# Performance work log

Measured on AMD Instinct MI355X. Metric: run time of the kernel, lower is better.

## Reference

```python
import jax, jax.numpy as jnp
import numpy as np

D = 128
N_ROUNDS = 8


def _lin(k, fan_in, fan_out):
    return jax.random.normal(k, (fan_in, fan_out), jnp.float32) * (1.0 / np.sqrt(fan_in)).astype(np.float32)


def setup_inputs() -> dict:
    key = jax.random.key(0)
    ks = jax.random.split(key, 10)
    n_vars, n_clauses, n_edges = 65536, 262144, 1048576
    n_lits = 2 * n_vars
    clause_index = jax.random.randint(ks[0], (n_edges,), 0, n_clauses)
    literal_index = jax.random.randint(ks[1], (n_edges,), 0, n_lits)
    return {
        "n_vars": n_vars,
        "n_clauses": n_clauses,
        "clause_index": clause_index,
        "literal_index": literal_index,
        "L_init_scale": jnp.float32(1.0 / np.sqrt(D)),
        "C_init_scale": jnp.float32(1.0 / np.sqrt(D)),
        "LC_scale": jnp.float32(0.1),
        "CL_scale": jnp.float32(0.1),
        # C update MLP: [C, LC_msgs] (2d) -> d -> d
        "C_W1": _lin(ks[2], 2 * D, D), "C_b1": jnp.zeros((D,), jnp.float32),
        "C_W2": _lin(ks[3], D, D),     "C_b2": jnp.zeros((D,), jnp.float32),
        # L update MLP: [L, CL_msgs, flip(L)] (3d) -> d -> d
        "L_W1": _lin(ks[4], 3 * D, D), "L_b1": jnp.zeros((D,), jnp.float32),
        "L_W2": _lin(ks[5], D, D),     "L_b2": jnp.zeros((D,), jnp.float32),
        # V score MLP: [L_pos, L_neg] (2d) -> d -> 1
        "V_W1": _lin(ks[6], 2 * D, D), "V_b1": jnp.zeros((D,), jnp.float32),
        "V_W2": _lin(ks[7], D, 1),     "V_b2": jnp.zeros((1,), jnp.float32),
    }


def _mlp(x, W1, b1, W2, b2):
    # 2-layer MLP, relu on hidden layer only
    return jnp.maximum(x @ W1 + b1, 0.0) @ W2 + b2


def reference(n_vars, n_clauses, clause_index, literal_index,
              L_init_scale, C_init_scale, LC_scale, CL_scale,
              C_W1, C_b1, C_W2, C_b2,
              L_W1, L_b1, L_W2, L_b2,
              V_W1, V_b1, V_W2, V_b2):
    d = C_W2.shape[1]
    n_lits = 2 * n_vars
    L0 = jnp.ones((n_lits, d), jnp.float32) * L_init_scale
    C0 = jnp.ones((n_clauses, d), jnp.float32) * C_init_scale

    def flip(Lm):
        # swap positive/negative literal embeddings per variable
        pl, ul = jnp.split(Lm.reshape(n_vars, 2 * d), 2, axis=1)
        return jnp.concatenate([ul, pl], axis=1).reshape(n_lits, d)

    def step(carry, _):
        L, C = carry
        # literal -> clause messages (gather + segment sum)
        LC_msgs = jax.ops.segment_sum(L[literal_index], clause_index,
                                      num_segments=n_clauses) * LC_scale
        C_new = _mlp(jnp.concatenate([C, LC_msgs], axis=-1),
                     C_W1, C_b1, C_W2, C_b2) + C  # res_layers
        # clause -> literal messages
        CL_msgs = jax.ops.segment_sum(C_new[clause_index], literal_index,
                                      num_segments=n_lits) * CL_scale
        L_new = _mlp(jnp.concatenate([L, CL_msgs, flip(L)], axis=-1),
                     L_W1, L_b1, L_W2, L_b2) + L  # res_layers
        return (L_new, C_new), None

    (L, C), _ = jax.lax.scan(step, (L0, C0), None, length=N_ROUNDS)
    V = L.reshape(n_vars, 2 * d)
    V_scores = _mlp(V, V_W1, V_b1, V_W2, V_b2)
    return V_scores[:, 0]  # pi_core_var_logits
```

## Files before the change

kernel.cpp:

```cpp
#include <hip/hip_runtime.h>
#include <cstddef>

#define D_    128
#define NV_   65536
#define NL_   131072
#define NC_   262144
#define NE_   1048576
#define NROUNDS_ 8

typedef __attribute__((ext_vector_type(4)))  short short4v;
typedef __attribute__((ext_vector_type(8)))  short short8v;
typedef __attribute__((ext_vector_type(16))) float f32x16;

__device__ __forceinline__ float4 f4_load(const float* p) { return *(const float4*)p; }
__device__ __forceinline__ void   f4_store(float* p, float4 v) { *(float4*)p = v; }
__device__ __forceinline__ float4 f4_zero() { return make_float4(0.f, 0.f, 0.f, 0.f); }
__device__ __forceinline__ float4 f4_add(float4 a, float4 b) {
    a.x += b.x; a.y += b.y; a.z += b.z; a.w += b.w; return a;
}
__device__ __forceinline__ float4 f4_scale(float4 a, float s) {
    a.x *= s; a.y *= s; a.z *= s; a.w *= s; return a;
}

__device__ __forceinline__ void micro_fma(const float4 a[4], const float4 w[4], float4 acc[4]) {
#pragma unroll
    for (int i = 0; i < 4; i++) {
        float4 av = a[i];
        acc[i].x += av.x * w[0].x; acc[i].x += av.y * w[1].x; acc[i].x += av.z * w[2].x; acc[i].x += av.w * w[3].x;
        acc[i].y += av.x * w[0].y; acc[i].y += av.y * w[1].y; acc[i].y += av.z * w[2].y; acc[i].y += av.w * w[3].y;
        acc[i].z += av.x * w[0].z; acc[i].z += av.y * w[1].z; acc[i].z += av.z * w[2].z; acc[i].z += av.w * w[3].z;
        acc[i].w += av.x * w[0].w; acc[i].w += av.y * w[1].w; acc[i].w += av.z * w[2].w; acc[i].w += av.w * w[3].w;
    }
}

template<int KD, bool FLIP>
__device__ __forceinline__ void layer1_to_H(float* Xs, float* Wcs,
        const float* __restrict__ W1, const float* __restrict__ b1, int t)
{
    const int tr = t >> 5, tc = t & 31;
    float4 acc[4];
    acc[0] = acc[1] = acc[2] = acc[3] = f4_zero();
#pragma unroll 1
    for (int kc = 0; kc < KD; kc += 32) {
        __syncthreads();
#pragma unroll
        for (int i = t; i < 1024; i += 256)
            ((float4*)Wcs)[i] = ((const float4*)W1)[kc * 32 + i];
        __syncthreads();
        const bool fl = FLIP && (kc >= 256);
        const int ab = fl ? (kc - 256) : kc;
#pragma unroll
        for (int k = 0; k < 32; k += 4) {
            float4 a[4], w[4];
#pragma unroll
            for (int i = 0; i < 4; i++) {
                int r = 4 * tr + i;
                if (fl) r ^= 1;
                a[i] = f4_load(Xs + r * 256 + ab + k);
            }
#pragma unroll
            for (int kk = 0; kk < 4; kk++)
                w[kk] = f4_load(Wcs + (k + kk) * 128 + 4 * tc);
            micro_fma(a, w, acc);
        }
    }
    float4 bv = f4_load(b1 + 4 * tc);
    __syncthreads();
#pragma unroll
    for (int i = 0; i < 4; i++) {
        float4 h;
        h.x = fmaxf(acc[i].x + bv.x, 0.f);
        h.y = fmaxf(acc[i].y + bv.y, 0.f);
        h.z = fmaxf(acc[i].z + bv.z, 0.f);
        h.w = fmaxf(acc[i].w + bv.w, 0.f);
        f4_store(Xs + (4 * tr + i) * 256 + 128 + 4 * tc, h);
    }
}

__device__ __forceinline__ unsigned short f2bf(float x) {
    unsigned u = __float_as_uint(x);
    u += 0x7fffu + ((u >> 16) & 1u);
    return (unsigned short)(u >> 16);
}
__device__ __forceinline__ float bf2f(unsigned short h) {
    return __uint_as_float(((unsigned)h) << 16);
}
__device__ __forceinline__ void split_bf(float x, unsigned short& h, unsigned short& l) {
    h = f2bf(x);
    l = f2bf(x - bf2f(h));
}
__device__ __forceinline__ void cvt4(const float4& a, short4v& h, short4v& l) {
    unsigned short h0,h1,h2,h3,l0,l1,l2,l3;
    split_bf(a.x,h0,l0); split_bf(a.y,h1,l1); split_bf(a.z,h2,l2); split_bf(a.w,h3,l3);
    h = (short4v){(short)h0,(short)h1,(short)h2,(short)h3};
    l = (short4v){(short)l0,(short)l1,(short)l2,(short)l3};
}
__device__ __forceinline__ void cvt8(const float4& a, const float4& b, short8v& h, short8v& l) {
    unsigned short h0,h1,h2,h3,h4,h5,h6,h7,l0,l1,l2,l3,l4,l5,l6,l7;
    split_bf(a.x,h0,l0); split_bf(a.y,h1,l1); split_bf(a.z,h2,l2); split_bf(a.w,h3,l3);
    split_bf(b.x,h4,l4); split_bf(b.y,h5,l5); split_bf(b.z,h6,l6); split_bf(b.w,h7,l7);
    h = (short8v){(short)h0,(short)h1,(short)h2,(short)h3,(short)h4,(short)h5,(short)h6,(short)h7};
    l = (short8v){(short)l0,(short)l1,(short)l2,(short)l3,(short)l4,(short)l5,(short)l6,(short)l7};
}

__device__ __forceinline__ int pswz(int r, int k) { return (r * 256 + k * 2) ^ ((r & 7) << 4); }

__global__ void pack_weights(const float* __restrict__ W, short* __restrict__ out, int K)
{
    int o = blockIdx.x * 256 + threadIdx.x;
    if (o >= 2 * K * 128) return;
    int i = o & 7;
    int g = o >> 3;
    int n  = g & 127;
    int kk = (g >> 7) & 3;
    int p  = (g >> 9) & 1;
    int c  = g >> 10;
    int k  = c * 32 + kk * 8 + i;
    float x = W[k * 128 + n];
    unsigned short h = f2bf(x);
    unsigned short v = p ? f2bf(x - bf2f(h)) : h;
    out[o] = (short)v;
}

__global__ void fill_kernel(float* __restrict__ L, float* __restrict__ C,
                            const float* __restrict__ lsp, const float* __restrict__ csp)
{
    const float ls = *lsp, cs = *csp;
    const size_t stride = (size_t)gridDim.x * blockDim.x;
    size_t i0 = (size_t)blockIdx.x * blockDim.x + threadIdx.x;
    const size_t nL = (size_t)NL_ * D_ / 4, nC = (size_t)NC_ * D_ / 4;
    float4 lv = make_float4(ls, ls, ls, ls), cv = make_float4(cs, cs, cs, cs);
    for (size_t i = i0; i < nL; i += stride) ((float4*)L)[i] = lv;
    for (size_t i = i0; i < nC; i += stride) ((float4*)C)[i] = cv;
}

__global__ void count_kernel(const int* __restrict__ ci, const int* __restrict__ li,
                             int* __restrict__ ccnt, int* __restrict__ lcnt)
{
    int e = blockIdx.x * 256 + threadIdx.x;
    if (e < NE_) {
        atomicAdd(&ccnt[ci[e]], 1);
        atomicAdd(&lcnt[li[e]], 1);
    }
}

__global__ void scan_block(const int* __restrict__ in, int* __restrict__ out,
                           int* __restrict__ bsum)
{
    __shared__ int sh[256];
    const int t = threadIdx.x;
    const int base = blockIdx.x * 1024 + t * 4;
    int v0 = in[base], v1 = in[base + 1], v2 = in[base + 2], v3 = in[base + 3];
    int s = v0 + v1 + v2 + v3;
    sh[t] = s;
    __syncthreads();
    for (int off = 1; off < 256; off <<= 1) {
        int y = (t >= off) ? sh[t - off] : 0;
        __syncthreads();
        sh[t] += y;
        __syncthreads();
    }
    int excl = sh[t] - s;
    out[base + 0] = excl;
    out[base + 1] = excl + v0;
    out[base + 2] = excl + v0 + v1;
    out[base + 3] = excl + v0 + v1 + v2;
    if (t == 255) bsum[blockIdx.x] = sh[255];
}

__global__ void scan_top(int* __restrict__ bs, int n)
{
    __shared__ int sh[256];
    const int t = threadIdx.x;
    int v = (t < n) ? bs[t] : 0;
    sh[t] = v;
    __syncthreads();
    for (int off = 1; off < 256; off <<= 1) {
        int y = (t >= off) ? sh[t - off] : 0;
        __syncthreads();
        sh[t] += y;
        __syncthreads();
    }
    if (t < n) bs[t] = sh[t] - v;
}

__global__ void scan_add(int* __restrict__ offs, const int* __restrict__ bs,
                         int* __restrict__ cur, int n, int total)
{
    int i = blockIdx.x * 256 + threadIdx.x;
    if (i < n) {
        int v = offs[i] + bs[i >> 10];
        offs[i] = v;
        cur[i] = v;
    }
    if (i == 0) offs[n] = total;
}

__global__ void fill_csr(const int* __restrict__ ci, const int* __restrict__ li,
                         int* __restrict__ ccur, int* __restrict__ lcur,
                         int* __restrict__ cedges, int* __restrict__ ledges)
{
    int e = blockIdx.x * 256 + threadIdx.x;
    if (e < NE_) {
        int c = ci[e], l = li[e];
        int p = atomicAdd(&ccur[c], 1); cedges[p] = l;
        int q = atomicAdd(&lcur[l], 1); ledges[q] = c;
    }
}

template<bool FLIP>
__global__ __launch_bounds__(256, 5) void update_mfma(
        float* __restrict__ Mat, const float* __restrict__ Src,
        const int* __restrict__ offs, const int* __restrict__ eidx,
        const short* __restrict__ Wp1, const float* __restrict__ b1,
        const short* __restrict__ Wp2, const float* __restrict__ b2,
        const float* __restrict__ scale_p)
{
    __shared__ __align__(16) unsigned char SM[32768];
    unsigned char* sm = SM;
    const int t = threadIdx.x;
    const int base = blockIdx.x * 32;
    const int lane = t & 63, w = t >> 6;
    const int rA = lane & 31;
    const int kg = lane >> 5;
    const int nB = w * 32 + rA;

    float4 sv[4];
#pragma unroll
    for (int j = 0; j < 4; ++j)
        sv[j] = ((const float4*)Mat)[(size_t)base * 32 + t + j * 256];

    float4 a0 = f4_zero(), a1 = f4_zero(), a2 = f4_zero(), a3 = f4_zero();
    const int gr = t >> 3, gs = t & 7;
    {
        const int row = base + gr;
        const int e0 = offs[row], e1 = offs[row + 1];
        int e = e0;
        for (; e + 1 < e1; e += 2) {
            const float* P = Src + (size_t)eidx[e] * 128 + gs * 16;
            const float* Q = Src + (size_t)eidx[e + 1] * 128 + gs * 16;
            float4 p0 = f4_load(P), p1 = f4_load(P + 4), p2 = f4_load(P + 8), p3 = f4_load(P + 12);
            float4 q0 = f4_load(Q), q1 = f4_load(Q + 4), q2 = f4_load(Q + 8), q3 = f4_load(Q + 12);
            a0 = f4_add(a0, p0); a1 = f4_add(a1, p1); a2 = f4_add(a2, p2); a3 = f4_add(a3, p3);
            a0 = f4_add(a0, q0); a1 = f4_add(a1, q1); a2 = f4_add(a2, q2); a3 = f4_add(a3, q3);
        }
        if (e < e1) {
            const float* P = Src + (size_t)eidx[e] * 128 + gs * 16;
            a0 = f4_add(a0, f4_load(P));
            a1 = f4_add(a1, f4_load(P + 4));
            a2 = f4_add(a2, f4_load(P + 8));
            a3 = f4_add(a3, f4_load(P + 12));
        }
    }

#pragma unroll
    for (int j = 0; j < 4; ++j) {
        int i = t + j * 256;
        int r = i >> 5, q = i & 31;
        short4v hv, lv;
        cvt4(sv[j], hv, lv);
        *(short4v*)(sm + pswz(r, 4 * q)) = hv;
        *(short4v*)(sm + 8192 + pswz(r, 4 * q)) = lv;
    }
    {
        const float sc = *scale_p;
        a0 = f4_scale(a0, sc); a1 = f4_scale(a1, sc);
        a2 = f4_scale(a2, sc); a3 = f4_scale(a3, sc);
        short8v mh0, ml0, mh1, ml1;
        cvt8(a0, a1, mh0, ml0);
        cvt8(a2, a3, mh1, ml1);
        const int k0 = 16 * gs;
        *(short8v*)(sm + 16384 + pswz(gr, k0))     = mh0;
        *(short8v*)(sm + 16384 + pswz(gr, k0 + 8)) = mh1;
        *(short8v*)(sm + 24576 + pswz(gr, k0))     = ml0;
        *(short8v*)(sm + 24576 + pswz(gr, k0 + 8)) = ml1;
    }
    __syncthreads();

    f32x16 c0, c1;
#pragma unroll
    for (int i = 0; i < 16; ++i) { c0[i] = 0.f; c1[i] = 0.f; }

#define MFMA_STEP(Wp, st, ka, ar, AB) do {                                          \
        short8v ah = *(const short8v*)(sm + (AB) + pswz((ar), (ka)));               \
        short8v al = *(const short8v*)(sm + (AB) + 8192 + pswz((ar), (ka)));        \
        const short* Wc = (Wp) + ((st) >> 1) * 8192;                                \
        const int kk = ((st) & 1) * 2 + kg;                                         \
        short8v bh = *(const short8v*)(Wc + ((size_t)(kk * 128 + nB)) * 8);         \
        short8v bl = *(const short8v*)(Wc + ((size_t)((4 + kk) * 128 + nB)) * 8);   \
        c0 = __builtin_amdgcn_mfma_f32_32x32x16_bf16(ah, bh, c0, 0, 0, 0);          \
        c1 = __builtin_amdgcn_mfma_f32_32x32x16_bf16(ah, bl, c1, 0, 0, 0);          \
        c1 = __builtin_amdgcn_mfma_f32_32x32x16_bf16(al, bh, c1, 0, 0, 0);          \
    } while (0)

#pragma unroll 2
    for (int st = 0; st < 8; ++st)
        MFMA_STEP(Wp1, st, st * 16 + kg * 8, rA, 0);
#pragma unroll 2
    for (int st = 8; st < 16; ++st)
        MFMA_STEP(Wp1, st, (st - 8) * 16 + kg * 8, rA, 16384);
    if (FLIP) {
#pragma unroll 2
        for (int st = 16; st < 24; ++st)
            MFMA_STEP(Wp1, st, (st - 16) * 16 + kg * 8, rA ^ 1, 0);
    }
    __syncthreads();

    {
        const float b = b1[nB];
#pragma unroll
        for (int i = 0; i < 16; ++i) {
            int row = (i & 3) + 8 * (i >> 2) + 4 * kg;
            float h = fmaxf(c0[i] + c1[i] + b, 0.f);
            unsigned short hh, hl;
            split_bf(h, hh, hl);
            *(short*)(sm + 16384 + pswz(row, nB)) = (short)hh;
            *(short*)(sm + 24576 + pswz(row, nB)) = (short)hl;
        }
    }
    __syncthreads();

    float res[16];
#pragma unroll
    for (int i = 0; i < 16; ++i) {
        int row = (i & 3) + 8 * (i >> 2) + 4 * kg;
        unsigned short sh = *(const unsigned short*)(sm + pswz(row, nB));
        unsigned short sl = *(const unsigned short*)(sm + 8192 + pswz(row, nB));
        res[i] = bf2f(sh) + bf2f(sl);
    }

#pragma unroll
    for (int i = 0; i < 16; ++i) { c0[i] = 0.f; c1[i] = 0.f; }
#pragma unroll 2
    for (int st = 0; st < 8; ++st)
        MFMA_STEP(Wp2, st, st * 16 + kg * 8, rA, 16384);
#undef MFMA_STEP

    {
        const float b = b2[nB];
#pragma unroll
        for (int i = 0; i < 16; ++i) {
            int row = (i & 3) + 8 * (i >> 2) + 4 * kg;
            size_t gi = (size_t)(base + row) * 128 + nB;
            Mat[gi] = c0[i] + c1[i] + b + res[i];
        }
    }
}

__global__ __launch_bounds__(256) void v_score(
        float* __restrict__ out, const float* __restrict__ Lmat,
        const float* __restrict__ W1, const float* __restrict__ b1,
        const float* __restrict__ W2, const float* __restrict__ b2)
{
    __shared__ float Xs[32 * 256];
    __shared__ float Wcs[32 * 128];
    const int t = threadIdx.x;
    const int base = blockIdx.x * 32;

#pragma unroll
    for (int i = t; i < 2048; i += 256)
        ((float4*)Xs)[i] = ((const float4*)Lmat)[(size_t)base * 64 + i];

    layer1_to_H<256, false>(Xs, Wcs, W1, b1, t);
    __syncthreads();
    if (t < 32) ((float4*)Wcs)[t] = ((const float4*)W2)[t];
    __syncthreads();

    const int r = t >> 3, s = t & 7;
    float sum = 0.f;
#pragma unroll
    for (int j = 0; j < 16; j++)
        sum += Xs[r * 256 + 128 + s * 16 + j] * Wcs[s * 16 + j];
    sum += __shfl_xor(sum, 1);
    sum += __shfl_xor(sum, 2);
    sum += __shfl_xor(sum, 4);
    if (s == 0) out[base + r] = sum + b2[0];
}

extern "C" void kernel_launch(void* const* d_in, const int* in_sizes, int n_in,
                              void* d_out, int out_size, void* d_ws, size_t ws_size,
                              hipStream_t stream)
{
    const int*   ci   = (const int*)d_in[2];
    const int*   li   = (const int*)d_in[3];
    const float* Lsc  = (const float*)d_in[4];
    const float* Csc  = (const float*)d_in[5];
    const float* LCsc = (const float*)d_in[6];
    const float* CLsc = (const float*)d_in[7];
    const float* C_W1 = (const float*)d_in[8];
    const float* C_b1 = (const float*)d_in[9];
    const float* C_W2 = (const float*)d_in[10];
    const float* C_b2 = (const float*)d_in[11];
    const float* L_W1 = (const float*)d_in[12];
    const float* L_b1 = (const float*)d_in[13];
    const float* L_W2 = (const float*)d_in[14];
    const float* L_b2 = (const float*)d_in[15];
    const float* V_W1 = (const float*)d_in[16];
    const float* V_b1 = (const float*)d_in[17];
    const float* V_W2 = (const float*)d_in[18];
    const float* V_b2 = (const float*)d_in[19];
    float* out = (float*)d_out;

    char* w = (char*)d_ws;
    float* Cmat  = (float*)w; w += (size_t)NC_ * D_ * 4;
    float* Lmat  = (float*)w; w += (size_t)NL_ * D_ * 4;
    int* coffs   = (int*)w;   w += (size_t)(NC_ + 1) * 4;
    int* ccur    = (int*)w;   w += (size_t)NC_ * 4;
    int* cedges  = (int*)w;   w += (size_t)NE_ * 4;
    int* loffs   = (int*)w;   w += (size_t)(NL_ + 1) * 4;
    int* lcur    = (int*)w;   w += (size_t)NL_ * 4;
    int* ledges  = (int*)w;   w += (size_t)NE_ * 4;
    int* bsumC   = (int*)w;   w += 256 * 4;
    int* bsumL   = (int*)w;   w += 256 * 4;
    short* WpC1  = (short*)w; w += (size_t)2 * 256 * 128 * 2;
    short* WpC2  = (short*)w; w += (size_t)2 * 128 * 128 * 2;
    short* WpL1  = (short*)w; w += (size_t)2 * 384 * 128 * 2;
    short* WpL2  = (short*)w; w += (size_t)2 * 128 * 128 * 2;

    hipMemsetAsync(ccur, 0, (size_t)NC_ * 4, stream);
    hipMemsetAsync(lcur, 0, (size_t)NL_ * 4, stream);

    pack_weights<<<(2 * 256 * 128) / 256, 256, 0, stream>>>(C_W1, WpC1, 256);
    pack_weights<<<(2 * 128 * 128) / 256, 256, 0, stream>>>(C_W2, WpC2, 128);
    pack_weights<<<(2 * 384 * 128) / 256, 256, 0, stream>>>(L_W1, WpL1, 384);
    pack_weights<<<(2 * 128 * 128) / 256, 256, 0, stream>>>(L_W2, WpL2, 128);

    fill_kernel<<<2048, 256, 0, stream>>>(Lmat, Cmat, Lsc, Csc);
    count_kernel<<<NE_ / 256, 256, 0, stream>>>(ci, li, ccur, lcur);

    scan_block<<<NC_ / 1024, 256, 0, stream>>>(ccur, coffs, bsumC);
    scan_top<<<1, 256, 0, stream>>>(bsumC, NC_ / 1024);
    scan_add<<<NC_ / 256, 256, 0, stream>>>(coffs, bsumC, ccur, NC_, NE_);

    scan_block<<<NL_ / 1024, 256, 0, stream>>>(lcur, loffs, bsumL);
    scan_top<<<1, 256, 0, stream>>>(bsumL, NL_ / 1024);
    scan_add<<<NL_ / 256, 256, 0, stream>>>(loffs, bsumL, lcur, NL_, NE_);

    fill_csr<<<NE_ / 256, 256, 0, stream>>>(ci, li, ccur, lcur, cedges, ledges);

    for (int r = 0; r < NROUNDS_; r++) {
        update_mfma<false><<<NC_ / 32, 256, 0, stream>>>(
            Cmat, Lmat, coffs, cedges, WpC1, C_b1, WpC2, C_b2, LCsc);
        update_mfma<true><<<NL_ / 32, 256, 0, stream>>>(
            Lmat, Cmat, loffs, ledges, WpL1, L_b1, WpL2, L_b2, CLsc);
    }
    v_score<<<NV_ / 32, 256, 0, stream>>>(out, Lmat, V_W1, V_b1, V_W2, V_b2);
}
```

Measured before the change: 2.853 ms.

## Unroll gather by four, prefetch MFMA weights two steps ahead, defer residual load

```diff
diff --git a/kernel.cpp b/kernel.cpp
--- a/kernel.cpp
+++ b/kernel.cpp
@@ -229,6 +229,9 @@
 #pragma unroll
     for (int j = 0; j < 4; ++j)
         sv[j] = ((const float4*)Mat)[(size_t)base * 32 + t + j * 256];
+    const float b1v = b1[nB];
+    const float b2v = b2[nB];
+    const float sc  = *scale_p;
 
     float4 a0 = f4_zero(), a1 = f4_zero(), a2 = f4_zero(), a3 = f4_zero();
     const int gr = t >> 3, gs = t & 7;
@@ -236,15 +239,21 @@
         const int row = base + gr;
         const int e0 = offs[row], e1 = offs[row + 1];
         int e = e0;
-        for (; e + 1 < e1; e += 2) {
-            const float* P = Src + (size_t)eidx[e] * 128 + gs * 16;
-            const float* Q = Src + (size_t)eidx[e + 1] * 128 + gs * 16;
-            float4 p0 = f4_load(P), p1 = f4_load(P + 4), p2 = f4_load(P + 8), p3 = f4_load(P + 12);
-            float4 q0 = f4_load(Q), q1 = f4_load(Q + 4), q2 = f4_load(Q + 8), q3 = f4_load(Q + 12);
-            a0 = f4_add(a0, p0); a1 = f4_add(a1, p1); a2 = f4_add(a2, p2); a3 = f4_add(a3, p3);
-            a0 = f4_add(a0, q0); a1 = f4_add(a1, q1); a2 = f4_add(a2, q2); a3 = f4_add(a3, q3);
+        for (; e + 3 < e1; e += 4) {
+            const float* P0 = Src + (size_t)eidx[e]     * 128 + gs * 16;
+            const float* P1 = Src + (size_t)eidx[e + 1] * 128 + gs * 16;
+            const float* P2 = Src + (size_t)eidx[e + 2] * 128 + gs * 16;
+            const float* P3 = Src + (size_t)eidx[e + 3] * 128 + gs * 16;
+            float4 u0 = f4_load(P0), u1 = f4_load(P0 + 4), u2 = f4_load(P0 + 8), u3 = f4_load(P0 + 12);
+            float4 v0 = f4_load(P1), v1 = f4_load(P1 + 4), v2 = f4_load(P1 + 8), v3 = f4_load(P1 + 12);
+            float4 w0 = f4_load(P2), w1 = f4_load(P2 + 4), w2 = f4_load(P2 + 8), w3 = f4_load(P2 + 12);
+            float4 x0 = f4_load(P3), x1 = f4_load(P3 + 4), x2 = f4_load(P3 + 8), x3 = f4_load(P3 + 12);
+            a0 = f4_add(a0, f4_add(f4_add(u0, v0), f4_add(w0, x0)));
+            a1 = f4_add(a1, f4_add(f4_add(u1, v1), f4_add(w1, x1)));
+            a2 = f4_add(a2, f4_add(f4_add(u2, v2), f4_add(w2, x2)));
+            a3 = f4_add(a3, f4_add(f4_add(u3, v3), f4_add(w3, x3)));
         }
-        if (e < e1) {
+        for (; e < e1; ++e) {
             const float* P = Src + (size_t)eidx[e] * 128 + gs * 16;
             a0 = f4_add(a0, f4_load(P));
             a1 = f4_add(a1, f4_load(P + 4));
@@ -263,7 +272,6 @@
         *(short4v*)(sm + 8192 + pswz(r, 4 * q)) = lv;
     }
     {
-        const float sc = *scale_p;
         a0 = f4_scale(a0, sc); a1 = f4_scale(a1, sc);
         a2 = f4_scale(a2, sc); a3 = f4_scale(a3, sc);
         short8v mh0, ml0, mh1, ml1;
@@ -281,69 +289,77 @@
 #pragma unroll
     for (int i = 0; i < 16; ++i) { c0[i] = 0.f; c1[i] = 0.f; }
 
-#define MFMA_STEP(Wp, st, ka, ar, AB) do {                                          \
-        short8v ah = *(const short8v*)(sm + (AB) + pswz((ar), (ka)));               \
-        short8v al = *(const short8v*)(sm + (AB) + 8192 + pswz((ar), (ka)));        \
-        const short* Wc = (Wp) + ((st) >> 1) * 8192;                                \
-        const int kk = ((st) & 1) * 2 + kg;                                         \
-        short8v bh = *(const short8v*)(Wc + ((size_t)(kk * 128 + nB)) * 8);         \
-        short8v bl = *(const short8v*)(Wc + ((size_t)((4 + kk) * 128 + nB)) * 8);   \
-        c0 = __builtin_amdgcn_mfma_f32_32x32x16_bf16(ah, bh, c0, 0, 0, 0);          \
-        c1 = __builtin_amdgcn_mfma_f32_32x32x16_bf16(ah, bl, c1, 0, 0, 0);          \
-        c1 = __builtin_amdgcn_mfma_f32_32x32x16_bf16(al, bh, c1, 0, 0, 0);          \
+#define LOADB(Wp, st, BH, BL) do {                                              \
+        const short* Wc_ = (Wp) + ((st) >> 1) * 8192;                           \
+        const int kk_ = ((st) & 1) * 2 + kg;                                    \
+        BH = *(const short8v*)(Wc_ + ((size_t)(kk_ * 128 + nB)) * 8);           \
+        BL = *(const short8v*)(Wc_ + ((size_t)((4 + kk_) * 128 + nB)) * 8);     \
     } while (0)
-
-#pragma unroll 2
-    for (int st = 0; st < 8; ++st)
-        MFMA_STEP(Wp1, st, st * 16 + kg * 8, rA, 0);
-#pragma unroll 2
-    for (int st = 8; st < 16; ++st)
-        MFMA_STEP(Wp1, st, (st - 8) * 16 + kg * 8, rA, 16384);
-    if (FLIP) {
-#pragma unroll 2
-        for (int st = 16; st < 24; ++st)
-            MFMA_STEP(Wp1, st, (st - 16) * 16 + kg * 8, rA ^ 1, 0);
-    }
-    __syncthreads();
+#define BH_SLOT(i) (((i) % 3 == 0) ? pbh0 : ((i) % 3 == 1) ? pbh1 : pbh2)
+#define BL_SLOT(i) (((i) % 3 == 0) ? pbl0 : ((i) % 3 == 1) ? pbl1 : pbl2)
+
+    short8v pbh0, pbl0, pbh1, pbl1, pbh2, pbl2;
 
     {
-        const float b = b1[nB];
-#pragma unroll
-        for (int i = 0; i < 16; ++i) {
-            int row = (i & 3) + 8 * (i >> 2) + 4 * kg;
-            float h = fmaxf(c0[i] + c1[i] + b, 0.f);
-            unsigned short hh, hl;
-            split_bf(h, hh, hl);
-            *(short*)(sm + 16384 + pswz(row, nB)) = (short)hh;
-            *(short*)(sm + 24576 + pswz(row, nB)) = (short)hl;
+        constexpr int NS1 = FLIP ? 24 : 16;
+        LOADB(Wp1, 0, pbh0, pbl0);
+        LOADB(Wp1, 1, pbh1, pbl1);
+#pragma unroll
+        for (int st = 0; st < NS1; ++st) {
+            if (st + 2 < NS1) LOADB(Wp1, st + 2, BH_SLOT(st + 2), BL_SLOT(st + 2));
+            const int AB = (st < 16) ? ((st < 8) ? 0 : 16384) : 0;
+            const int ar = (st < 16) ? rA : (rA ^ 1);
+            const int ka = (st & 7) * 16 + kg * 8;
+            short8v ah = *(const short8v*)(sm + AB + pswz(ar, ka));
+            short8v al = *(const short8v*)(sm + AB + 8192 + pswz(ar, ka));
+            short8v bh = BH_SLOT(st), bl = BL_SLOT(st);
+            c0 = __builtin_amdgcn_mfma_f32_32x32x16_bf16(ah, bh, c0, 0, 0, 0);
+            c1 = __builtin_amdgcn_mfma_f32_32x32x16_bf16(ah, bl, c1, 0, 0, 0);
+            c1 = __builtin_amdgcn_mfma_f32_32x32x16_bf16(al, bh, c1, 0, 0, 0);
         }
     }
     __syncthreads();
 
-    float res[16];
 #pragma unroll
     for (int i = 0; i < 16; ++i) {
         int row = (i & 3) + 8 * (i >> 2) + 4 * kg;
-        unsigned short sh = *(const unsigned short*)(sm + pswz(row, nB));
-        unsigned short sl = *(const unsigned short*)(sm + 8192 + pswz(row, nB));
-        res[i] = bf2f(sh) + bf2f(sl);
-    }
+        float h = fmaxf(c0[i] + c1[i] + b1v, 0.f);
+        unsigned short hh, hl;
+        split_bf(h, hh, hl);
+        *(short*)(sm + 16384 + pswz(row, nB)) = (short)hh;
+        *(short*)(sm + 24576 + pswz(row, nB)) = (short)hl;
+    }
+    __syncthreads();
 
 #pragma unroll
     for (int i = 0; i < 16; ++i) { c0[i] = 0.f; c1[i] = 0.f; }
-#pragma unroll 2
-    for (int st = 0; st < 8; ++st)
-        MFMA_STEP(Wp2, st, st * 16 + kg * 8, rA, 16384);
-#undef MFMA_STEP
-
     {
-        const float b = b2[nB];
-#pragma unroll
-        for (int i = 0; i < 16; ++i) {
-            int row = (i & 3) + 8 * (i >> 2) + 4 * kg;
-            size_t gi = (size_t)(base + row) * 128 + nB;
-            Mat[gi] = c0[i] + c1[i] + b + res[i];
+        LOADB(Wp2, 0, pbh0, pbl0);
+        LOADB(Wp2, 1, pbh1, pbl1);
+#pragma unroll
+        for (int st = 0; st < 8; ++st) {
+            if (st + 2 < 8) LOADB(Wp2, st + 2, BH_SLOT(st + 2), BL_SLOT(st + 2));
+            const int ka = st * 16 + kg * 8;
+            short8v ah = *(const short8v*)(sm + 16384 + pswz(rA, ka));
+            short8v al = *(const short8v*)(sm + 24576 + pswz(rA, ka));
+            short8v bh = BH_SLOT(st), bl = BL_SLOT(st);
+            c0 = __builtin_amdgcn_mfma_f32_32x32x16_bf16(ah, bh, c0, 0, 0, 0);
+            c1 = __builtin_amdgcn_mfma_f32_32x32x16_bf16(ah, bl, c1, 0, 0, 0);
+            c1 = __builtin_amdgcn_mfma_f32_32x32x16_bf16(al, bh, c1, 0, 0, 0);
         }
+    }
+#undef LOADB
+#undef BH_SLOT
+#undef BL_SLOT
+
+#pragma unroll
+    for (int i = 0; i < 16; ++i) {
+        int row = (i & 3) + 8 * (i >> 2) + 4 * kg;
+        unsigned short shh = *(const unsigned short*)(sm + pswz(row, nB));
+        unsigned short sll = *(const unsigned short*)(sm + 8192 + pswz(row, nB));
+        float res = bf2f(shh) + bf2f(sll);
+        size_t gi = (size_t)(base + row) * 128 + nB;
+        Mat[gi] = c0[i] + c1[i] + b2v + res;
     }
 }
 
```

After: 3.123 ms. +9.5%, slower.
